# Kernel optimization log

Measured on AMD Instinct MI355X. Metric: run time of the kernel, lower is better.

The kernel has to match this reference:

```python
import jax, jax.numpy as jnp
import numpy as np

LOG2 = float(np.log(2.0))

def ssp(x):
    # shifted softplus: log(0.5*exp(x) + 0.5)
    return jax.nn.softplus(x) - LOG2


def setup_inputs() -> dict:
    B, A, N = 8, 512, 64
    n_atom, n_spatial, n_filters = 256, 128, 256
    n_ang_feat = 2 * 2 * 2 * 8 * 2  # 2*n_zetas*2*n_angular*n_zetas = 128
    key = jax.random.key(0)
    ks = jax.random.split(key, 16)
    f32 = jnp.float32
    inp = {
        'x': jax.random.normal(ks[0], (B, A, n_atom), f32),
        'r_ij': jax.random.uniform(ks[1], (B, A, N), f32) * 6.0,  # some beyond cutoff=5
        'f_ij': jax.random.normal(ks[2], (B, A, N, n_spatial), f32),
        'G_i': jax.random.normal(ks[3], (B, A, n_ang_feat), f32),
        'neighbor_mask': jnp.ones((B, A, N), f32),
        'neighbors': jax.random.randint(ks[4], (B, A, N), 0, A),
        # CFConv params: in2f (no bias), filter MLP, f2out
        'W_in2f': jax.random.normal(ks[5], (n_atom, n_filters), f32) * (n_atom ** -0.5),
        'W1': jax.random.normal(ks[6], (n_spatial, n_filters), f32) * (n_spatial ** -0.5),
        'b1': jnp.zeros((n_filters,), f32),
        'W2': jax.random.normal(ks[7], (n_filters, n_filters), f32) * (n_filters ** -0.5),
        'b2': jnp.zeros((n_filters,), f32),
        'W_f2out': jax.random.normal(ks[8], (n_filters, n_atom), f32) * (n_filters ** -0.5),
        'b_f2out': jnp.zeros((n_atom,), f32),
        # post-cfconv dense and angular dense (no bias)
        'W_dense': jax.random.normal(ks[9], (n_atom, n_atom), f32) * (n_atom ** -0.5),
        'b_dense': jnp.zeros((n_atom,), f32),
        'W_ang': jax.random.normal(ks[10], (n_ang_feat, n_atom), f32) * (n_ang_feat ** -0.5),
    }
    return inp


def reference(x, r_ij, f_ij, G_i, neighbor_mask, neighbors,
              W_in2f, W1, b1, W2, b2, W_f2out, b_f2out,
              W_dense, b_dense, W_ang):
    cutoff = 5.0
    # filter-generating MLP on distance expansion: [B,A,N,n_filters]
    W = ssp(jnp.einsum('bans,sf->banf', f_ij, W1) + b1)
    W = jnp.einsum('banf,fg->bang', W, W2) + b2
    # hard cutoff mask on distances
    C = (r_ij <= cutoff).astype(W.dtype)
    W = W * C[..., None]
    # in2f projection then neighbor gather
    xf = jnp.einsum('bad,df->baf', x, W_in2f)  # [B,A,F]
    B, A, F = xf.shape
    N = neighbors.shape[-1]
    y = jnp.take_along_axis(xf, neighbors.reshape(B, A * N, 1), axis=1)
    y = y.reshape(B, A, N, F)
    # elementwise filter, mask padded neighbors, sum-aggregate over neighbors
    y = (y * W * neighbor_mask[..., None]).sum(axis=2)  # [B,A,F]
    v_rad = jnp.einsum('baf,fd->bad', y, W_f2out) + b_f2out
    v_rad = jnp.einsum('bad,de->bae', v_rad, W_dense) + b_dense
    v_ang = jnp.einsum('bag,gd->bad', G_i, W_ang)
    return ssp(v_rad + v_ang)
```

## Files before the change

### kernel.cpp

```cpp
#include <hip/hip_runtime.h>


typedef __bf16 bf16x8 __attribute__((ext_vector_type(8)));
typedef __bf16 bf16x2 __attribute__((ext_vector_type(2)));
typedef float f32x4 __attribute__((ext_vector_type(4)));
typedef int i32x4 __attribute__((ext_vector_type(4)));
typedef unsigned short u16;
typedef unsigned int u32;

#define LDA 136
#define LDH 264

#define O_WIN 1048576
#define O_W1  1114112
#define O_W2  1146880
#define O_WF  1212416
#define O_WD  1277952
#define O_WA  1343488
#define O_Y   1376256
#define WS_NEED ((size_t)(2424832) * 2)

#define X_WF 98304
#define X_WD 163840
#define X_WA 229376

static __device__ __forceinline__ float b2f(u16 u) {
  union { float f; u32 i; } v; v.i = ((u32)u) << 16; return v.f;
}
static __device__ __forceinline__ float b2f_lo(u32 p) {
  union { float f; u32 i; } v; v.i = p << 16; return v.f;
}
static __device__ __forceinline__ float b2f_hi(u32 p) {
  union { float f; u32 i; } v; v.i = p & 0xffff0000u; return v.f;
}
static __device__ __forceinline__ u32 pk2(float lo, float hi) {
  bf16x2 v; v[0] = (__bf16)lo; v[1] = (__bf16)hi;
  return __builtin_bit_cast(u32, v);
}
static __device__ __forceinline__ float sspf(float x) {
  float t = __expf(fminf(x, 60.0f));
  return __logf(fmaf(t, 0.5f, 0.5f));
}
static __device__ __forceinline__ bf16x8 ldfrag(const u16* p) {
  return __builtin_bit_cast(bf16x8, *(const uint4*)p);
}
static __device__ __forceinline__ float ldsc(const u16* p, bool fm, size_t i) {
  return fm ? ((const float*)p)[i] : b2f(p[i]);
}

static __device__ __forceinline__ void pack_strip(
    const u16* __restrict__ W, bool fm, int q, int KC, u16* __restrict__ dst, u16* T) {
  int tid = threadIdx.x;
  if (fm) {
    const float* src = (const float*)W + (size_t)q * 32 * 256;
#pragma unroll
    for (int i = 0; i < 8; i++) {
      int c = tid + 256 * i;
      int row = c >> 6, col4 = (c & 63) * 4;
      float4 v = *(const float4*)(src + (size_t)row * 256 + col4);
      uint2 o; o.x = pk2(v.x, v.y); o.y = pk2(v.z, v.w);
      *(uint2*)(T + row * LDH + col4) = o;
    }
  } else {
    const u16* src = W + (size_t)q * 32 * 256;
#pragma unroll
    for (int i = 0; i < 8; i++) {
      int c = tid + 256 * i;
      int row = c >> 6, col4 = (c & 63) * 4;
      *(uint2*)(T + row * LDH + col4) = *(const uint2*)(src + (size_t)row * 256 + col4);
    }
  }
  __syncthreads();
#pragma unroll
  for (int i = 0; i < 4; i++) {
    int idx = tid + 256 * i;
    int flane = idx & 63, c = idx >> 6;
    int col = (c >> 2) * 64 + (flane & 15) * 4 + (c & 3);
    int r0 = (flane >> 4) * 8;
    u32 t0 = (u32)T[(r0 + 0) * LDH + col] | ((u32)T[(r0 + 1) * LDH + col] << 16);
    u32 t1 = (u32)T[(r0 + 2) * LDH + col] | ((u32)T[(r0 + 3) * LDH + col] << 16);
    u32 t2 = (u32)T[(r0 + 4) * LDH + col] | ((u32)T[(r0 + 5) * LDH + col] << 16);
    u32 t3 = (u32)T[(r0 + 6) * LDH + col] | ((u32)T[(r0 + 7) * LDH + col] << 16);
    uint4 o; o.x = t0; o.y = t1; o.z = t2; o.w = t3;
    *(uint4*)(dst + ((size_t)(c * KC + q) * 64 + flane) * 8) = o;
  }
}

__global__ __launch_bounds__(256) void pack6(
    const u16* __restrict__ Win, const u16* __restrict__ W1, const u16* __restrict__ W2,
    const u16* __restrict__ Wf, const u16* __restrict__ Wd, const u16* __restrict__ Wa,
    const u16* __restrict__ nm, u16* __restrict__ base) {
  __shared__ __align__(16) u16 T[32 * LDH];
  bool fm = (nm[0] == 0);
  int b = blockIdx.x;
  if (b < 8)       pack_strip(Win, fm, b,      8, base + O_WIN, T);
  else if (b < 12) pack_strip(W1,  fm, b - 8,  4, base + O_W1,  T);
  else if (b < 20) pack_strip(W2,  fm, b - 12, 8, base + O_W2,  T);
  else if (b < 28) pack_strip(Wf,  fm, b - 20, 8, base + O_WF,  T);
  else if (b < 36) pack_strip(Wd,  fm, b - 28, 8, base + O_WD,  T);
  else             pack_strip(Wa,  fm, b - 36, 4, base + O_WA,  T);
}

__global__ __launch_bounds__(256) void pack_a(
    const u16* __restrict__ Win, const u16* __restrict__ W1, const u16* __restrict__ W2,
    const u16* __restrict__ nm, u16* __restrict__ outb) {
  __shared__ __align__(16) u16 T[32 * LDH];
  bool fm = (nm[0] == 0);
  int b = blockIdx.x;
  if (b < 8)       pack_strip(Win, fm, b,      8, outb + O_WIN, T);
  else if (b < 12) pack_strip(W1,  fm, b - 8,  4, outb + O_W1,  T);
  else             pack_strip(W2,  fm, b - 12, 8, outb + O_W2,  T);
}

__global__ __launch_bounds__(256) void pack_b(
    const u16* __restrict__ Wf, const u16* __restrict__ Wd, const u16* __restrict__ Wa,
    const u16* __restrict__ nm, u16* __restrict__ dst) {
  __shared__ __align__(16) u16 T[32 * LDH];
  bool fm = (nm[0] == 0);
  int b = blockIdx.x;
  if (b < 8)       pack_strip(Wf, fm, b,      8, dst + X_WF, T);
  else if (b < 16) pack_strip(Wd, fm, b - 8,  8, dst + X_WD, T);
  else             pack_strip(Wa, fm, b - 16, 4, dst + X_WA, T);
}

__global__ __launch_bounds__(256) void k1_xf(
    const u16* __restrict__ x, const u16* __restrict__ nm,
    const u16* __restrict__ winp, u16* __restrict__ xfout) {
  __shared__ __align__(16) u16 sX[16 * LDH];
  bool fm = (nm[0] == 0);
  int bid = blockIdx.x, tid = threadIdx.x;
  int w = tid >> 6, lane = tid & 63, quad = lane >> 4, l16 = lane & 15;
  if (fm) {
    const float* src = (const float*)x + (size_t)bid * 2048;
    int c = tid;
    float4 a = *(const float4*)(src + c * 8), b = *(const float4*)(src + c * 8 + 4);
    uint4 o; o.x = pk2(a.x, a.y); o.y = pk2(a.z, a.w);
    o.z = pk2(b.x, b.y); o.w = pk2(b.z, b.w);
    *(uint4*)(sX + (c >> 5) * LDH + (c & 31) * 8) = o;
  } else {
    const u16* src = x + (size_t)bid * 2048;
    int c = tid;
    *(uint4*)(sX + (c >> 5) * LDH + (c & 31) * 8) = *(const uint4*)(src + c * 8);
  }
  __syncthreads();
  f32x4 acc[4];
#pragma unroll
  for (int ct = 0; ct < 4; ct++) acc[ct] = (f32x4){0.f, 0.f, 0.f, 0.f};
#pragma unroll
  for (int q = 0; q < 8; q++) {
    bf16x8 af = ldfrag(sX + l16 * LDH + q * 32 + quad * 8);
    bf16x8 bfr[4];
#pragma unroll
    for (int ct = 0; ct < 4; ct++)
      bfr[ct] = ldfrag(winp + ((size_t)((w * 4 + ct) * 8 + q) * 64 + lane) * 8);
#pragma unroll
    for (int ct = 0; ct < 4; ct++)
      acc[ct] = __builtin_amdgcn_mfma_f32_16x16x32_bf16(af, bfr[ct], acc[ct], 0, 0, 0);
  }
  if (quad < 2) {
#pragma unroll
    for (int r = 0; r < 4; r++) {
      uint2 o; o.x = pk2(acc[0][r], acc[1][r]); o.y = pk2(acc[2][r], acc[3][r]);
      *(uint2*)(xfout + (size_t)(bid * 8 + quad * 4 + r) * 256 + w * 64 + l16 * 4) = o;
    }
  }
}

__global__ __launch_bounds__(256, 3) void k2_main(
    const u16* __restrict__ fij, const u16* __restrict__ rij, const u16* __restrict__ nm,
    const int* __restrict__ nbr, const u16* __restrict__ b1, const u16* __restrict__ b2,
    const u16* __restrict__ xf, const u16* __restrict__ w1p, const u16* __restrict__ w2p,
    u16* __restrict__ yout, int ystr) {
  __shared__ __align__(16) u16 sF[64 * LDA];
  __shared__ __align__(16) u16 sH[64 * LDH];
  __shared__ __align__(16) float cm[128];
  __shared__ __align__(16) int nb[128];
  bool fm = (nm[0] == 0);
  int bid = blockIdx.x, tid = threadIdx.x;
  int w = tid >> 6, lane = tid & 63, quad = lane >> 4, l16 = lane & 15;
  int t0 = bid * 2;

  if (tid < 128) {
    float r = ldsc(rij, fm, (size_t)t0 * 64 + tid);
    float m = ldsc(nm, fm, (size_t)t0 * 64 + tid);
    cm[tid] = (r <= 5.0f) ? m : 0.0f;
    nb[tid] = nbr[t0 * 64 + tid];
  }

  if (fm) {
    const float* fsrc = (const float*)fij + (size_t)t0 * 8192;
#pragma unroll
    for (int i = 0; i < 4; i++) {
      int c = tid + 256 * i;
      const float* p = fsrc + c * 8;
      float4 a = *(const float4*)p, b = *(const float4*)(p + 4);
      uint4 o; o.x = pk2(a.x, a.y); o.y = pk2(a.z, a.w);
      o.z = pk2(b.x, b.y); o.w = pk2(b.z, b.w);
      *(uint4*)(sF + (c >> 4) * LDA + (c & 15) * 8) = o;
    }
  } else {
    const u16* fsrc = fij + (size_t)t0 * 8192;
#pragma unroll
    for (int i = 0; i < 4; i++) {
      int c = tid + 256 * i;
      *(uint4*)(sF + (c >> 4) * LDA + (c & 15) * 8) = *(const uint4*)(fsrc + c * 8);
    }
  }
  __syncthreads();

  f32x4 zero = {0.f, 0.f, 0.f, 0.f};
  uint4 sr0, sr1, sr2, sr3, sr4, sr5, sr6, sr7;

#pragma unroll
  for (int t = 0; t < 2; t++) {
    int tt = t0 + t;

    if (t == 0) {
      if (fm) {
        const float* fsrc = (const float*)fij + (size_t)(tt + 1) * 8192;
        const float* p0 = fsrc + (tid + 0) * 8;
        const float* p1 = fsrc + (tid + 256) * 8;
        const float* p2 = fsrc + (tid + 512) * 8;
        const float* p3 = fsrc + (tid + 768) * 8;
        sr0 = *(const uint4*)p0; sr1 = *(const uint4*)(p0 + 4);
        sr2 = *(const uint4*)p1; sr3 = *(const uint4*)(p1 + 4);
        sr4 = *(const uint4*)p2; sr5 = *(const uint4*)(p2 + 4);
        sr6 = *(const uint4*)p3; sr7 = *(const uint4*)(p3 + 4);
      } else {
        const u16* fsrc = fij + (size_t)(tt + 1) * 8192;
        sr0 = *(const uint4*)(fsrc + (tid + 0) * 8);
        sr1 = *(const uint4*)(fsrc + (tid + 256) * 8);
        sr2 = *(const uint4*)(fsrc + (tid + 512) * 8);
        sr3 = *(const uint4*)(fsrc + (tid + 768) * 8);
      }
    }

    f32x4 acc[4][4];
#pragma unroll
    for (int mt = 0; mt < 4; mt++)
#pragma unroll
      for (int ct = 0; ct < 4; ct++) acc[mt][ct] = zero;
#pragma unroll
    for (int q = 0; q < 4; q++) {
      bf16x8 af[4], bfr[4];
#pragma unroll
      for (int mt = 0; mt < 4; mt++)
        af[mt] = ldfrag(sF + (mt * 16 + l16) * LDA + q * 32 + quad * 8);
#pragma unroll
      for (int ct = 0; ct < 4; ct++)
        bfr[ct] = ldfrag(w1p + ((size_t)((w * 4 + ct) * 4 + q) * 64 + lane) * 8);
#pragma unroll
      for (int mt = 0; mt < 4; mt++)
#pragma unroll
        for (int ct = 0; ct < 4; ct++)
          acc[mt][ct] = __builtin_amdgcn_mfma_f32_16x16x32_bf16(af[mt], bfr[ct], acc[mt][ct], 0, 0, 0);
    }

    float bb1[4];
    if (fm) {
      float4 v = *(const float4*)((const float*)b1 + w * 64 + l16 * 4);
      bb1[0] = v.x; bb1[1] = v.y; bb1[2] = v.z; bb1[3] = v.w;
    } else {
      uint2 v = *(const uint2*)(b1 + w * 64 + l16 * 4);
      bb1[0] = b2f_lo(v.x); bb1[1] = b2f_hi(v.x); bb1[2] = b2f_lo(v.y); bb1[3] = b2f_hi(v.y);
    }
#pragma unroll
    for (int mt = 0; mt < 4; mt++)
#pragma unroll
      for (int r = 0; r < 4; r++) {
        int m = mt * 16 + quad * 4 + r;
        uint2 o;
        o.x = pk2(sspf(acc[mt][0][r] + bb1[0]), sspf(acc[mt][1][r] + bb1[1]));
        o.y = pk2(sspf(acc[mt][2][r] + bb1[2]), sspf(acc[mt][3][r] + bb1[3]));
        *(uint2*)(sH + m * LDH + w * 64 + l16 * 4) = o;
      }
    __syncthreads();

    if (t == 0) {
      if (fm) {
#pragma unroll
        for (int i = 0; i < 4; i++) {
          int c = tid + 256 * i;
          float4 a, b;
          switch (i) {
            case 0: a = __builtin_bit_cast(float4, sr0); b = __builtin_bit_cast(float4, sr1); break;
            case 1: a = __builtin_bit_cast(float4, sr2); b = __builtin_bit_cast(float4, sr3); break;
            case 2: a = __builtin_bit_cast(float4, sr4); b = __builtin_bit_cast(float4, sr5); break;
            default: a = __builtin_bit_cast(float4, sr6); b = __builtin_bit_cast(float4, sr7); break;
          }
          uint4 o; o.x = pk2(a.x, a.y); o.y = pk2(a.z, a.w);
          o.z = pk2(b.x, b.y); o.w = pk2(b.z, b.w);
          *(uint4*)(sF + (c >> 4) * LDA + (c & 15) * 8) = o;
        }
      } else {
#pragma unroll
        for (int i = 0; i < 4; i++) {
          int c = tid + 256 * i;
          uint4 o;
          switch (i) {
            case 0: o = sr0; break;
            case 1: o = sr1; break;
            case 2: o = sr2; break;
            default: o = sr3; break;
          }
          *(uint4*)(sF + (c >> 4) * LDA + (c & 15) * 8) = o;
        }
      }
    }

    f32x4 acc2[4][4];
#pragma unroll
    for (int mt = 0; mt < 4; mt++)
#pragma unroll
      for (int ct = 0; ct < 4; ct++) acc2[mt][ct] = zero;
#pragma unroll
    for (int q = 0; q < 8; q++) {
      bf16x8 af[4], bfr[4];
#pragma unroll
      for (int mt = 0; mt < 4; mt++)
        af[mt] = ldfrag(sH + (mt * 16 + l16) * LDH + q * 32 + quad * 8);
#pragma unroll
      for (int ct = 0; ct < 4; ct++)
        bfr[ct] = ldfrag(w2p + ((size_t)((w * 4 + ct) * 8 + q) * 64 + lane) * 8);
#pragma unroll
      for (int mt = 0; mt < 4; mt++)
#pragma unroll
        for (int ct = 0; ct < 4; ct++)
          acc2[mt][ct] = __builtin_amdgcn_mfma_f32_16x16x32_bf16(af[mt], bfr[ct], acc2[mt][ct], 0, 0, 0);
    }

    float bb2[4];
    if (fm) {
      float4 v = *(const float4*)((const float*)b2 + w * 64 + l16 * 4);
      bb2[0] = v.x; bb2[1] = v.y; bb2[2] = v.z; bb2[3] = v.w;
    } else {
      uint2 v = *(const uint2*)(b2 + w * 64 + l16 * 4);
      bb2[0] = b2f_lo(v.x); bb2[1] = b2f_hi(v.x); bb2[2] = b2f_lo(v.y); bb2[3] = b2f_hi(v.y);
    }
    const u16* xcol = xf + (size_t)((tt >> 9) * 512) * 256 + w * 64 + l16 * 4;
    float s0 = 0.f, s1 = 0.f, s2 = 0.f, s3 = 0.f;
#pragma unroll
    for (int mt = 0; mt < 4; mt++) {
      i32x4 nbv = *(const i32x4*)(nb + t * 64 + mt * 16 + quad * 4);
      f32x4 cv = *(const f32x4*)(cm + t * 64 + mt * 16 + quad * 4);
#pragma unroll
      for (int r = 0; r < 4; r++) {
        uint2 v = *(const uint2*)(xcol + (size_t)nbv[r] * 256);
        float c = cv[r];
        s0 = fmaf((acc2[mt][0][r] + bb2[0]) * c, b2f_lo(v.x), s0);
        s1 = fmaf((acc2[mt][1][r] + bb2[1]) * c, b2f_hi(v.x), s1);
        s2 = fmaf((acc2[mt][2][r] + bb2[2]) * c, b2f_lo(v.y), s2);
        s3 = fmaf((acc2[mt][3][r] + bb2[3]) * c, b2f_hi(v.y), s3);
      }
    }
    s0 += __shfl_xor(s0, 16); s0 += __shfl_xor(s0, 32);
    s1 += __shfl_xor(s1, 16); s1 += __shfl_xor(s1, 32);
    s2 += __shfl_xor(s2, 16); s2 += __shfl_xor(s2, 32);
    s3 += __shfl_xor(s3, 16); s3 += __shfl_xor(s3, 32);
    if (quad == 0) {
      uint2 o; o.x = pk2(s0, s1); o.y = pk2(s2, s3);
      *(uint2*)(yout + (size_t)tt * ystr + w * 64 + l16 * 4) = o;
    }
    if (t == 0) __syncthreads();
  }
}

__global__ __launch_bounds__(512) void k3_out(
    const u16* __restrict__ y, int ystr, const u16* __restrict__ G,
    const u16* __restrict__ bf2, const u16* __restrict__ bd, const u16* __restrict__ nm,
    const u16* __restrict__ wfp, const u16* __restrict__ wdp, const u16* __restrict__ wap,
    u16* __restrict__ outb) {
  __shared__ __align__(16) u16 sY[16 * LDH];
  __shared__ __align__(16) u16 sH2[16 * LDH];
  __shared__ __align__(16) u16 sG[16 * LDA];
  bool fm = (nm[0] == 0);
  int bid = blockIdx.x, tid = threadIdx.x;
  int cg = tid >> 6, lane = tid & 63, quad = lane >> 4, l16 = lane & 15;
  int f0 = (cg >> 1) * 64 + l16 * 4 + (cg & 1) * 2;
  {
    int c = tid;
    const u16* src = y + (size_t)(bid * 16 + (c >> 5)) * ystr + (c & 31) * 8;
    *(uint4*)(sY + (c >> 5) * LDH + (c & 31) * 8) = *(const uint4*)src;
  }
  if (fm) {
    if (tid < 256) {
      int c = tid;
      const float* p = (const float*)G + (size_t)(bid * 16 + (c >> 4)) * 128 + (c & 15) * 8;
      float4 a = *(const float4*)p, b = *(const float4*)(p + 4);
      uint4 o; o.x = pk2(a.x, a.y); o.y = pk2(a.z, a.w);
      o.z = pk2(b.x, b.y); o.w = pk2(b.z, b.w);
      *(uint4*)(sG + (c >> 4) * LDA + (c & 15) * 8) = o;
    }
  } else {
    if (tid < 256) {
      int c = tid;
      *(uint4*)(sG + (c >> 4) * LDA + (c & 15) * 8) =
          *(const uint4*)(G + (size_t)(bid * 16 + (c >> 4)) * 128 + (c & 15) * 8);
    }
  }
  __syncthreads();
  f32x4 zero = {0.f, 0.f, 0.f, 0.f};
  f32x4 acc[2];
  acc[0] = zero; acc[1] = zero;
#pragma unroll
  for (int q = 0; q < 8; q++) {
    bf16x8 af = ldfrag(sY + l16 * LDH + q * 32 + quad * 8);
    bf16x8 bfr[2];
#pragma unroll
    for (int ct = 0; ct < 2; ct++)
      bfr[ct] = ldfrag(wfp + ((size_t)((cg * 2 + ct) * 8 + q) * 64 + lane) * 8);
#pragma unroll
    for (int ct = 0; ct < 2; ct++)
      acc[ct] = __builtin_amdgcn_mfma_f32_16x16x32_bf16(af, bfr[ct], acc[ct], 0, 0, 0);
  }
  float bm0, bm1;
  if (fm) {
    float2 t = *(const float2*)((const float*)bf2 + f0);
    bm0 = t.x; bm1 = t.y;
  } else {
    u32 t = *(const u32*)(bf2 + f0);
    bm0 = b2f_lo(t); bm1 = b2f_hi(t);
  }
#pragma unroll
  for (int r = 0; r < 4; r++) {
    int m = quad * 4 + r;
    *(u32*)(sH2 + m * LDH + f0) = pk2(acc[0][r] + bm0, acc[1][r] + bm1);
  }
  __syncthreads();
  acc[0] = zero; acc[1] = zero;
#pragma unroll
  for (int q = 0; q < 8; q++) {
    bf16x8 af = ldfrag(sH2 + l16 * LDH + q * 32 + quad * 8);
    bf16x8 bfr[2];
#pragma unroll
    for (int ct = 0; ct < 2; ct++)
      bfr[ct] = ldfrag(wdp + ((size_t)((cg * 2 + ct) * 8 + q) * 64 + lane) * 8);
#pragma unroll
    for (int ct = 0; ct < 2; ct++)
      acc[ct] = __builtin_amdgcn_mfma_f32_16x16x32_bf16(af, bfr[ct], acc[ct], 0, 0, 0);
  }
#pragma unroll
  for (int q = 0; q < 4; q++) {
    bf16x8 af = ldfrag(sG + l16 * LDA + q * 32 + quad * 8);
    bf16x8 bfr[2];
#pragma unroll
    for (int ct = 0; ct < 2; ct++)
      bfr[ct] = ldfrag(wap + ((size_t)((cg * 2 + ct) * 4 + q) * 64 + lane) * 8);
#pragma unroll
    for (int ct = 0; ct < 2; ct++)
      acc[ct] = __builtin_amdgcn_mfma_f32_16x16x32_bf16(af, bfr[ct], acc[ct], 0, 0, 0);
  }
  float bd0, bd1;
  if (fm) {
    float2 t = *(const float2*)((const float*)bd + f0);
    bd0 = t.x; bd1 = t.y;
  } else {
    u32 t = *(const u32*)(bd + f0);
    bd0 = b2f_lo(t); bd1 = b2f_hi(t);
  }
  float* out32 = (float*)outb;
#pragma unroll
  for (int r = 0; r < 4; r++) {
    size_t row = (size_t)bid * 16 + quad * 4 + r;
    float v0 = sspf(acc[0][r] + bd0);
    float v1 = sspf(acc[1][r] + bd1);
    if (fm) {
      float2 o; o.x = v0; o.y = v1;
      *(float2*)(out32 + row * 256 + f0) = o;
    } else {
      *(u32*)(outb + row * 256 + f0) = pk2(v0, v1);
    }
  }
}

extern "C" void kernel_launch(void* const* d_in, const int* in_sizes, int n_in,
                              void* d_out, int out_size, void* d_ws, size_t ws_size,
                              hipStream_t stream) {
  u16*       x    = (u16*)d_in[0];
  const u16* rij  = (const u16*)d_in[1];
  u16*       fij  = (u16*)d_in[2];
  const u16* Gi   = (const u16*)d_in[3];
  const u16* nmsk = (const u16*)d_in[4];
  const int* nbr  = (const int*)d_in[5];
  const u16* Win  = (const u16*)d_in[6];
  const u16* W1   = (const u16*)d_in[7];
  const u16* b1   = (const u16*)d_in[8];
  const u16* W2   = (const u16*)d_in[9];
  const u16* b2   = (const u16*)d_in[10];
  const u16* Wf   = (const u16*)d_in[11];
  const u16* bf2  = (const u16*)d_in[12];
  const u16* Wd   = (const u16*)d_in[13];
  const u16* bd   = (const u16*)d_in[14];
  const u16* Wa   = (const u16*)d_in[15];
  u16* out = (u16*)d_out;

  bool fmh = (in_sizes[1] == 8 * 512 * 64 * 4);
  bool usews = (ws_size >= WS_NEED) && (d_ws != nullptr);

  if (usews) {
    u16* ws = (u16*)d_ws;
    pack6<<<40, 256, 0, stream>>>(Win, W1, W2, Wf, Wd, Wa, nmsk, ws);
    k1_xf<<<512, 256, 0, stream>>>(x, nmsk, ws + O_WIN, ws);
    k2_main<<<2048, 256, 0, stream>>>(fij, rij, nmsk, nbr, b1, b2,
                                      ws, ws + O_W1, ws + O_W2, ws + O_Y, 256);
    k3_out<<<256, 512, 0, stream>>>(ws + O_Y, 256, Gi, bf2, bd, nmsk,
                                    ws + O_WF, ws + O_WD, ws + O_WA, out);
  } else {
    int ystr = fmh ? 16384 : 8192;
    pack_a<<<20, 256, 0, stream>>>(Win, W1, W2, nmsk, out);
    k1_xf<<<512, 256, 0, stream>>>(x, nmsk, out + O_WIN, out);
    pack_b<<<20, 256, 0, stream>>>(Wf, Wd, Wa, nmsk, x);
    k2_main<<<2048, 256, 0, stream>>>(fij, rij, nmsk, nbr, b1, b2,
                                      out, out + O_W1, out + O_W2, fij, ystr);
    k3_out<<<256, 512, 0, stream>>>(fij, ystr, Gi, bf2, bd, nmsk,
                                    x + X_WF, x + X_WD, x + X_WA, out);
  }
}
```

Before: 292.2 us.

## Split k2_main filter columns across eight waves with 512-thread blocks

Doubles the k2_main block from 256 to 512 threads, so each of eight waves owns 32 filter columns instead of 64. Per-wave accumulators, B fragments and prefetch registers are halved. This lowers register pressure and raises waves per CU to hide gather and MFMA latency. In exchange, every wave now reloads the same A fragments from LDS for half the MFMA work, which doubles LDS read traffic per block, and the gather loads shrink to 4-byte accesses.

New measurement: 295.2 us. Within noise of the previous version (+1.0%).

```diff
diff --git a/kernel.cpp b/kernel.cpp
--- a/kernel.cpp
+++ b/kernel.cpp
@@ -166,7 +166,7 @@
   }
 }
 
-__global__ __launch_bounds__(256, 3) void k2_main(
+__global__ __launch_bounds__(512, 4) void k2_main(
     const u16* __restrict__ fij, const u16* __restrict__ rij, const u16* __restrict__ nm,
     const int* __restrict__ nbr, const u16* __restrict__ b1, const u16* __restrict__ b2,
     const u16* __restrict__ xf, const u16* __restrict__ w1p, const u16* __restrict__ w2p,
@@ -178,6 +178,7 @@
   bool fm = (nm[0] == 0);
   int bid = blockIdx.x, tid = threadIdx.x;
   int w = tid >> 6, lane = tid & 63, quad = lane >> 4, l16 = lane & 15;
+  int f0 = (w >> 1) * 64 + l16 * 4 + (w & 1) * 2;
   int t0 = bid * 2;
 
   if (tid < 128) {
@@ -190,8 +191,8 @@
   if (fm) {
     const float* fsrc = (const float*)fij + (size_t)t0 * 8192;
 #pragma unroll
-    for (int i = 0; i < 4; i++) {
-      int c = tid + 256 * i;
+    for (int i = 0; i < 2; i++) {
+      int c = tid + 512 * i;
       const float* p = fsrc + c * 8;
       float4 a = *(const float4*)p, b = *(const float4*)(p + 4);
       uint4 o; o.x = pk2(a.x, a.y); o.y = pk2(a.z, a.w);
@@ -201,15 +202,15 @@
   } else {
     const u16* fsrc = fij + (size_t)t0 * 8192;
 #pragma unroll
-    for (int i = 0; i < 4; i++) {
-      int c = tid + 256 * i;
+    for (int i = 0; i < 2; i++) {
+      int c = tid + 512 * i;
       *(uint4*)(sF + (c >> 4) * LDA + (c & 15) * 8) = *(const uint4*)(fsrc + c * 8);
     }
   }
   __syncthreads();
 
   f32x4 zero = {0.f, 0.f, 0.f, 0.f};
-  uint4 sr0, sr1, sr2, sr3, sr4, sr5, sr6, sr7;
+  uint4 sr0, sr1, sr2, sr3;
 
 #pragma unroll
   for (int t = 0; t < 2; t++) {
@@ -218,149 +219,123 @@
     if (t == 0) {
       if (fm) {
         const float* fsrc = (const float*)fij + (size_t)(tt + 1) * 8192;
-        const float* p0 = fsrc + (tid + 0) * 8;
-        const float* p1 = fsrc + (tid + 256) * 8;
-        const float* p2 = fsrc + (tid + 512) * 8;
-        const float* p3 = fsrc + (tid + 768) * 8;
+        const float* p0 = fsrc + tid * 8;
+        const float* p1 = fsrc + (tid + 512) * 8;
         sr0 = *(const uint4*)p0; sr1 = *(const uint4*)(p0 + 4);
         sr2 = *(const uint4*)p1; sr3 = *(const uint4*)(p1 + 4);
-        sr4 = *(const uint4*)p2; sr5 = *(const uint4*)(p2 + 4);
-        sr6 = *(const uint4*)p3; sr7 = *(const uint4*)(p3 + 4);
       } else {
         const u16* fsrc = fij + (size_t)(tt + 1) * 8192;
-        sr0 = *(const uint4*)(fsrc + (tid + 0) * 8);
-        sr1 = *(const uint4*)(fsrc + (tid + 256) * 8);
-        sr2 = *(const uint4*)(fsrc + (tid + 512) * 8);
-        sr3 = *(const uint4*)(fsrc + (tid + 768) * 8);
+        sr0 = *(const uint4*)(fsrc + tid * 8);
+        sr1 = *(const uint4*)(fsrc + (tid + 512) * 8);
       }
     }
 
-    f32x4 acc[4][4];
+    f32x4 acc[4][2];
 #pragma unroll
     for (int mt = 0; mt < 4; mt++)
 #pragma unroll
-      for (int ct = 0; ct < 4; ct++) acc[mt][ct] = zero;
+      for (int ct = 0; ct < 2; ct++) acc[mt][ct] = zero;
 #pragma unroll
     for (int q = 0; q < 4; q++) {
-      bf16x8 af[4], bfr[4];
+      bf16x8 af[4], bfr[2];
 #pragma unroll
       for (int mt = 0; mt < 4; mt++)
         af[mt] = ldfrag(sF + (mt * 16 + l16) * LDA + q * 32 + quad * 8);
 #pragma unroll
-      for (int ct = 0; ct < 4; ct++)
-        bfr[ct] = ldfrag(w1p + ((size_t)((w * 4 + ct) * 4 + q) * 64 + lane) * 8);
+      for (int ct = 0; ct < 2; ct++)
+        bfr[ct] = ldfrag(w1p + ((size_t)((w * 2 + ct) * 4 + q) * 64 + lane) * 8);
 #pragma unroll
       for (int mt = 0; mt < 4; mt++)
 #pragma unroll
-        for (int ct = 0; ct < 4; ct++)
+        for (int ct = 0; ct < 2; ct++)
           acc[mt][ct] = __builtin_amdgcn_mfma_f32_16x16x32_bf16(af[mt], bfr[ct], acc[mt][ct], 0, 0, 0);
     }
 
-    float bb1[4];
+    float bb1[2];
     if (fm) {
-      float4 v = *(const float4*)((const float*)b1 + w * 64 + l16 * 4);
-      bb1[0] = v.x; bb1[1] = v.y; bb1[2] = v.z; bb1[3] = v.w;
+      float2 v = *(const float2*)((const float*)b1 + f0);
+      bb1[0] = v.x; bb1[1] = v.y;
     } else {
-      uint2 v = *(const uint2*)(b1 + w * 64 + l16 * 4);
-      bb1[0] = b2f_lo(v.x); bb1[1] = b2f_hi(v.x); bb1[2] = b2f_lo(v.y); bb1[3] = b2f_hi(v.y);
+      u32 v = *(const u32*)(b1 + f0);
+      bb1[0] = b2f_lo(v); bb1[1] = b2f_hi(v);
     }
 #pragma unroll
     for (int mt = 0; mt < 4; mt++)
 #pragma unroll
       for (int r = 0; r < 4; r++) {
         int m = mt * 16 + quad * 4 + r;
-        uint2 o;
-        o.x = pk2(sspf(acc[mt][0][r] + bb1[0]), sspf(acc[mt][1][r] + bb1[1]));
-        o.y = pk2(sspf(acc[mt][2][r] + bb1[2]), sspf(acc[mt][3][r] + bb1[3]));
-        *(uint2*)(sH + m * LDH + w * 64 + l16 * 4) = o;
+        *(u32*)(sH + m * LDH + f0) =
+            pk2(sspf(acc[mt][0][r] + bb1[0]), sspf(acc[mt][1][r] + bb1[1]));
       }
     __syncthreads();
 
     if (t == 0) {
       if (fm) {
 #pragma unroll
-        for (int i = 0; i < 4; i++) {
-          int c = tid + 256 * i;
-          float4 a, b;
-          switch (i) {
-            case 0: a = __builtin_bit_cast(float4, sr0); b = __builtin_bit_cast(float4, sr1); break;
-            case 1: a = __builtin_bit_cast(float4, sr2); b = __builtin_bit_cast(float4, sr3); break;
-            case 2: a = __builtin_bit_cast(float4, sr4); b = __builtin_bit_cast(float4, sr5); break;
-            default: a = __builtin_bit_cast(float4, sr6); b = __builtin_bit_cast(float4, sr7); break;
-          }
+        for (int i = 0; i < 2; i++) {
+          int c = tid + 512 * i;
+          float4 a = __builtin_bit_cast(float4, i ? sr2 : sr0);
+          float4 b = __builtin_bit_cast(float4, i ? sr3 : sr1);
           uint4 o; o.x = pk2(a.x, a.y); o.y = pk2(a.z, a.w);
           o.z = pk2(b.x, b.y); o.w = pk2(b.z, b.w);
           *(uint4*)(sF + (c >> 4) * LDA + (c & 15) * 8) = o;
         }
       } else {
 #pragma unroll
-        for (int i = 0; i < 4; i++) {
-          int c = tid + 256 * i;
-          uint4 o;
-          switch (i) {
-            case 0: o = sr0; break;
-            case 1: o = sr1; break;
-            case 2: o = sr2; break;
-            default: o = sr3; break;
-          }
-          *(uint4*)(sF + (c >> 4) * LDA + (c & 15) * 8) = o;
+        for (int i = 0; i < 2; i++) {
+          int c = tid + 512 * i;
+          *(uint4*)(sF + (c >> 4) * LDA + (c & 15) * 8) = i ? sr1 : sr0;
         }
       }
     }
 
-    f32x4 acc2[4][4];
+    f32x4 acc2[4][2];
 #pragma unroll
     for (int mt = 0; mt < 4; mt++)
 #pragma unroll
-      for (int ct = 0; ct < 4; ct++) acc2[mt][ct] = zero;
+      for (int ct = 0; ct < 2; ct++) acc2[mt][ct] = zero;
 #pragma unroll
     for (int q = 0; q < 8; q++) {
-      bf16x8 af[4], bfr[4];
+      bf16x8 af[4], bfr[2];
 #pragma unroll
       for (int mt = 0; mt < 4; mt++)
         af[mt] = ldfrag(sH + (mt * 16 + l16) * LDH + q * 32 + quad * 8);
 #pragma unroll
-      for (int ct = 0; ct < 4; ct++)
-        bfr[ct] = ldfrag(w2p + ((size_t)((w * 4 + ct) * 8 + q) * 64 + lane) * 8);
+      for (int ct = 0; ct < 2; ct++)
+        bfr[ct] = ldfrag(w2p + ((size_t)((w * 2 + ct) * 8 + q) * 64 + lane) * 8);
 #pragma unroll
       for (int mt = 0; mt < 4; mt++)
 #pragma unroll
-        for (int ct = 0; ct < 4; ct++)
+        for (int ct = 0; ct < 2; ct++)
           acc2[mt][ct] = __builtin_amdgcn_mfma_f32_16x16x32_bf16(af[mt], bfr[ct], acc2[mt][ct], 0, 0, 0);
     }
 
-    float bb2[4];
+    float bb2[2];
     if (fm) {
-      float4 v = *(const float4*)((const float*)b2 + w * 64 + l16 * 4);
-      bb2[0] = v.x; bb2[1] = v.y; bb2[2] = v.z; bb2[3] = v.w;
+      float2 v = *(const float2*)((const float*)b2 + f0);
+      bb2[0] = v.x; bb2[1] = v.y;
     } else {
-      uint2 v = *(const uint2*)(b2 + w * 64 + l16 * 4);
-      bb2[0] = b2f_lo(v.x); bb2[1] = b2f_hi(v.x); bb2[2] = b2f_lo(v.y); bb2[3] = b2f_hi(v.y);
-    }
-    const u16* xcol = xf + (size_t)((tt >> 9) * 512) * 256 + w * 64 + l16 * 4;
-    float s0 = 0.f, s1 = 0.f, s2 = 0.f, s3 = 0.f;
+      u32 v = *(const u32*)(b2 + f0);
+      bb2[0] = b2f_lo(v); bb2[1] = b2f_hi(v);
+    }
+    const u16* xcol = xf + (size_t)((tt >> 9) * 512) * 256 + f0;
+    float s0 = 0.f, s1 = 0.f;
 #pragma unroll
     for (int mt = 0; mt < 4; mt++) {
       i32x4 nbv = *(const i32x4*)(nb + t * 64 + mt * 16 + quad * 4);
       f32x4 cv = *(const f32x4*)(cm + t * 64 + mt * 16 + quad * 4);
 #pragma unroll
       for (int r = 0; r < 4; r++) {
-        uint2 v = *(const uint2*)(xcol + (size_t)nbv[r] * 256);
+        u32 v = *(const u32*)(xcol + (size_t)nbv[r] * 256);
         float c = cv[r];
-        s0 = fmaf((acc2[mt][0][r] + bb2[0]) * c, b2f_lo(v.x), s0);
-        s1 = fmaf((acc2[mt][1][r] + bb2[1]) * c, b2f_hi(v.x), s1);
-        s2 = fmaf((acc2[mt][2][r] + bb2[2]) * c, b2f_lo(v.y), s2);
-        s3 = fmaf((acc2[mt][3][r] + bb2[3]) * c, b2f_hi(v.y), s3);
+        s0 = fmaf((acc2[mt][0][r] + bb2[0]) * c, b2f_lo(v), s0);
+        s1 = fmaf((acc2[mt][1][r] + bb2[1]) * c, b2f_hi(v), s1);
       }
     }
     s0 += __shfl_xor(s0, 16); s0 += __shfl_xor(s0, 32);
     s1 += __shfl_xor(s1, 16); s1 += __shfl_xor(s1, 32);
-    s2 += __shfl_xor(s2, 16); s2 += __shfl_xor(s2, 32);
-    s3 += __shfl_xor(s3, 16); s3 += __shfl_xor(s3, 32);
-    if (quad == 0) {
-      uint2 o; o.x = pk2(s0, s1); o.y = pk2(s2, s3);
-      *(uint2*)(yout + (size_t)tt * ystr + w * 64 + l16 * 4) = o;
-    }
+    if (quad == 0)
+      *(u32*)(yout + (size_t)tt * ystr + f0) = pk2(s0, s1);
     if (t == 0) __syncthreads();
   }
 }
@@ -501,7 +476,7 @@
     u16* ws = (u16*)d_ws;
     pack6<<<40, 256, 0, stream>>>(Win, W1, W2, Wf, Wd, Wa, nmsk, ws);
     k1_xf<<<512, 256, 0, stream>>>(x, nmsk, ws + O_WIN, ws);
-    k2_main<<<2048, 256, 0, stream>>>(fij, rij, nmsk, nbr, b1, b2,
+    k2_main<<<2048, 512, 0, stream>>>(fij, rij, nmsk, nbr, b1, b2,
                                       ws, ws + O_W1, ws + O_W2, ws + O_Y, 256);
     k3_out<<<256, 512, 0, stream>>>(ws + O_Y, 256, Gi, bf2, bd, nmsk,
                                     ws + O_WF, ws + O_WD, ws + O_WA, out);
@@ -510,7 +485,7 @@
     pack_a<<<20, 256, 0, stream>>>(Win, W1, W2, nmsk, out);
     k1_xf<<<512, 256, 0, stream>>>(x, nmsk, out + O_WIN, out);
     pack_b<<<20, 256, 0, stream>>>(Wf, Wd, Wa, nmsk, x);
-    k2_main<<<2048, 256, 0, stream>>>(fij, rij, nmsk, nbr, b1, b2,
+    k2_main<<<2048, 512, 0, stream>>>(fij, rij, nmsk, nbr, b1, b2,
                                       out, out + O_W1, out + O_W2, fij, ystr);
     k3_out<<<256, 512, 0, stream>>>(fij, ystr, Gi, bf2, bd, nmsk,
                                     x + X_WF, x + X_WD, x + X_WA, out);
```
